# Optimization experiments

Measured on AMD Instinct MI355X. Metric: run time of the kernel, lower is better.

Reference implementation:

```python
import jax, jax.numpy as jnp
import numpy as np

B, T, H, W, C = 2, 8, 64, 64, 128
NH, KT, KH, KW = 4, 3, 7, 7
HD = C // NH
SCALE = HD ** -0.5


def _starts(L, ks):
    i = jnp.arange(L)
    return jnp.clip(i - ks // 2, 0, L - ks)  # NATTEN border-clamped window start


def _na3d(q, k, v, rpb):
    # q,k,v: [B,T,H,W,NH,HD]; rpb: [NH,2KT-1,2KH-1,2KW-1]
    st, sh, sw = _starts(T, KT), _starts(H, KH), _starts(W, KW)
    ot, oh, ow = jnp.meshgrid(jnp.arange(KT), jnp.arange(KH), jnp.arange(KW), indexing='ij')
    ot, oh, ow = ot.ravel(), oh.ravel(), ow.ravel()          # [K] kernel offsets, K=KT*KH*KW
    t_abs = st[None, :] + ot[:, None]                        # [K,T] absolute neighbor coords
    h_abs = sh[None, :] + oh[:, None]                        # [K,H]
    w_abs = sw[None, :] + ow[:, None]                        # [K,W]
    qs = q * SCALE
    it, ih, iw = jnp.arange(T), jnp.arange(H), jnp.arange(W)

    def score_step(_, idx):
        ta, ha, wa = idx
        kg = k[:, ta][:, :, ha][:, :, :, wa]                 # [B,T,H,W,NH,HD] shifted keys
        s = jnp.einsum('bthwnd,bthwnd->bthwn', qs, kg)
        rt = ta - it + (KT - 1)
        rh = ha - ih + (KH - 1)
        rw = wa - iw + (KW - 1)
        bias = rpb[:, rt][:, :, rh][:, :, :, rw]             # [NH,T,H,W]
        return None, s + jnp.transpose(bias, (1, 2, 3, 0))[None]

    _, scores = jax.lax.scan(score_step, None, (t_abs, h_abs, w_abs))  # [K,B,T,H,W,NH]
    attn = jax.nn.softmax(scores, axis=0)

    def av_step(acc, xs):
        a, ta, ha, wa = xs
        vg = v[:, ta][:, :, ha][:, :, :, wa]                 # [B,T,H,W,NH,HD]
        return acc + a[..., None] * vg, None

    out, _ = jax.lax.scan(av_step, jnp.zeros_like(q), (attn, t_abs, h_abs, w_abs))
    return out


def setup_inputs() -> dict:
    key = jax.random.key(0)
    ks = jax.random.split(key, 6)
    x = jax.random.normal(ks[0], (B, T, H, W, C), jnp.float32)
    y = jax.random.normal(ks[1], (B, T, H, W, C), jnp.float32)
    qv_w = jax.random.normal(ks[2], (C, 2 * C), jnp.float32) * 0.02
    qv_b = jnp.zeros((2 * C,), jnp.float32)
    k_w = jax.random.normal(ks[3], (C, C), jnp.float32) * 0.02
    k_b = jnp.zeros((C,), jnp.float32)
    proj_w = jax.random.normal(ks[4], (C, C), jnp.float32) * 0.02
    proj_b = jnp.zeros((C,), jnp.float32)
    rpb = jax.random.normal(ks[5], (NH, 2 * KT - 1, 2 * KH - 1, 2 * KW - 1), jnp.float32) * 0.02
    return {'x': x, 'y': y, 'qv_w': qv_w, 'qv_b': qv_b, 'k_w': k_w, 'k_b': k_b,
            'proj_w': proj_w, 'proj_b': proj_b, 'rpb': rpb}


def reference(x, y, qv_w, qv_b, k_w, k_b, proj_w, proj_b, rpb):
    qv = (x @ qv_w + qv_b).reshape(B, T, H, W, 2, NH, HD)
    q, v = qv[..., 0, :, :], qv[..., 1, :, :]
    k = (y @ k_w + k_b).reshape(B, T, H, W, NH, HD)
    o = _na3d(q, k, v, rpb).reshape(B, T, H, W, C)
    return o @ proj_w + proj_b
```

## Files before the change

kernel.cpp:

```cpp
#include <hip/hip_runtime.h>
#include <hip/hip_bf16.h>
#include <hip/hip_fp16.h>
#include <cmath>

#define Bv   2
#define Tv   8
#define Hv   64
#define Wv   64
#define MPOS (Bv*Tv*Hv*Wv)
#define SCALEv 0.17677669529663687f

#define SPOS  196
#define SVT   464
#define NCOLS 232

#define KOFF   0
#define VTOFF  13312
#define POFF   28160
#define RPBOFF 57856
#define INVOFF 61248
#define SCROFF 61504
#define SMEM_BYTES 69696

#define KPAD 136

typedef __attribute__((ext_vector_type(8))) short bf16x8;
typedef __attribute__((ext_vector_type(4))) float f32x4;

__device__ __forceinline__ unsigned short f2bf16(float x) {
  return __builtin_bit_cast(unsigned short, __float2bfloat16(x));
}
__device__ __forceinline__ float bf2f(unsigned short h) {
  return __uint_as_float((unsigned)h << 16);
}
__device__ __forceinline__ float h2f(unsigned short h) {
  return __half2float(__builtin_bit_cast(__half, h));
}
__device__ __forceinline__ unsigned short f2h(float x) {
  return __builtin_bit_cast(unsigned short, __float2half(x));
}
__device__ __forceinline__ unsigned pk2(float a, float b) {
  return (unsigned)f2bf16(a) | ((unsigned)f2bf16(b) << 16);
}
__device__ __forceinline__ void gload_lds16(const void* gsrc, void* ldst) {
  __builtin_amdgcn_global_load_lds(
      (const __attribute__((address_space(1))) unsigned int*)gsrc,
      (__attribute__((address_space(3))) unsigned int*)ldst, 16, 0, 0);
}

__global__ __launch_bounds__(256) void preconvert(
    const float* __restrict__ qv_w, const float* __restrict__ k_w,
    const float* __restrict__ proj_w,
    ushort* __restrict__ wqvT, ushort* __restrict__ wkT,
    ushort* __restrict__ wpT_hi, ushort* __restrict__ wpT_lo) {
  const int id = blockIdx.x * 256 + threadIdx.x;
  if (id < 32768) {
    const int n = id >> 7, kk = id & 127;
    wqvT[n * KPAD + kk] = f2bf16(qv_w[kk * 256 + n]);
  } else if (id < 49152) {
    const int j = id - 32768;
    const int n = j >> 7, kk = j & 127;
    wkT[n * KPAD + kk] = f2bf16(k_w[kk * 128 + n]);
  } else {
    const int j = id - 49152;
    const int n = j >> 7, kk = j & 127;
    const float v = proj_w[kk * 128 + n];
    const unsigned short hi = f2bf16(v);
    wpT_hi[n * KPAD + kk] = hi;
    wpT_lo[n * KPAD + kk] = f2bf16(v - bf2f(hi));
  }
}

__global__ __launch_bounds__(512) void gemm_qvk(
    const float* __restrict__ x, const float* __restrict__ y,
    const ushort* __restrict__ wqvT, const ushort* __restrict__ wkT,
    const float* __restrict__ qv_b, const float* __restrict__ k_b,
    ushort* __restrict__ qbuf, ushort* __restrict__ vbuf,
    ushort* __restrict__ kbuf) {
  __shared__ ushort Ws[128 * KPAD];
  const int tid  = threadIdx.x;
  const int bx   = blockIdx.x;
  const int seg  = bx >> 9;
  const int row0 = (bx & 511) * 128;

  const float*  A    = (seg == 2) ? y : x;
  const ushort* W    = (seg == 0) ? wqvT : (seg == 1) ? wqvT + 128 * KPAD : wkT;
  const float*  bias = (seg == 0) ? qv_b : (seg == 1) ? qv_b + 128 : k_b;
  ushort*       outp = (seg == 0) ? qbuf : (seg == 1) ? vbuf : kbuf;
  const float   scale = (seg == 0) ? SCALEv : 1.0f;

  {
    const uint4* wg = (const uint4*)W;
    for (int i = tid; i < 2176; i += 512)
      gload_lds16(wg + i, (uint4*)Ws + i);
  }

  const int wv = tid >> 6, lane = tid & 63, quad = lane >> 4, l16 = lane & 15;
  const int arow = row0 + wv * 16 + l16;

  bf16x8 af[4];
#pragma unroll
  for (int kk = 0; kk < 4; ++kk) {
    const float4* ap = (const float4*)(A + (size_t)arow * 128 + kk * 32 + quad * 8);
    const float4 a = ap[0], b2 = ap[1];
    af[kk] = __builtin_bit_cast(bf16x8,
        make_uint4(pk2(a.x, a.y), pk2(a.z, a.w), pk2(b2.x, b2.y), pk2(b2.z, b2.w)));
  }
  __syncthreads();

  f32x4 C[8];
#pragma unroll
  for (int nt = 0; nt < 8; ++nt) C[nt] = (f32x4){0.f, 0.f, 0.f, 0.f};

#pragma unroll
  for (int kk = 0; kk < 4; ++kk) {
#pragma unroll
    for (int nt = 0; nt < 8; ++nt) {
      const bf16x8 b2 = *(const bf16x8*)(Ws + (nt * 16 + l16) * KPAD + kk * 32 + quad * 8);
      C[nt] = __builtin_amdgcn_mfma_f32_16x16x32_bf16(af[kk], b2, C[nt], 0, 0, 0);
    }
  }

#pragma unroll
  for (int nt = 0; nt < 8; ++nt) {
    const int col = nt * 16 + l16;
    const float bv = bias[col];
#pragma unroll
    for (int r2 = 0; r2 < 4; ++r2) {
      const size_t row = row0 + wv * 16 + quad * 4 + r2;
      outp[row * 128 + col] = f2bf16((C[nt][r2] + bv) * scale);
    }
  }
}

__global__ __launch_bounds__(512) void gemm_proj_mfma(
    const float* __restrict__ o, const ushort* __restrict__ wpT_hi,
    const ushort* __restrict__ wpT_lo, const float* __restrict__ proj_b,
    float* __restrict__ out) {
  __shared__ ushort Wh[128 * KPAD];
  __shared__ ushort Wl[128 * KPAD];
  const int tid  = threadIdx.x;
  const int row0 = blockIdx.x * 128;
  {
    const uint4* wgh = (const uint4*)wpT_hi;
    const uint4* wgl = (const uint4*)wpT_lo;
    for (int i = tid; i < 2176; i += 512) {
      gload_lds16(wgh + i, (uint4*)Wh + i);
      gload_lds16(wgl + i, (uint4*)Wl + i);
    }
  }

  const int wv = tid >> 6, lane = tid & 63, quad = lane >> 4, l16 = lane & 15;
  const int arow = row0 + wv * 16 + l16;

  bf16x8 ah[4], al[4];
#pragma unroll
  for (int kk = 0; kk < 4; ++kk) {
    const float4* ap = (const float4*)(o + (size_t)arow * 128 + kk * 32 + quad * 8);
    const float4 a = ap[0], b2 = ap[1];
    const float vs[8] = {a.x, a.y, a.z, a.w, b2.x, b2.y, b2.z, b2.w};
    unsigned hw[4], lw[4];
#pragma unroll
    for (int e = 0; e < 4; ++e) {
      const unsigned short h0 = f2bf16(vs[2 * e]);
      const unsigned short h1 = f2bf16(vs[2 * e + 1]);
      hw[e] = (unsigned)h0 | ((unsigned)h1 << 16);
      lw[e] = (unsigned)f2bf16(vs[2 * e] - bf2f(h0)) |
              ((unsigned)f2bf16(vs[2 * e + 1] - bf2f(h1)) << 16);
    }
    ah[kk] = __builtin_bit_cast(bf16x8, make_uint4(hw[0], hw[1], hw[2], hw[3]));
    al[kk] = __builtin_bit_cast(bf16x8, make_uint4(lw[0], lw[1], lw[2], lw[3]));
  }
  __syncthreads();

  f32x4 C[8];
#pragma unroll
  for (int nt = 0; nt < 8; ++nt) C[nt] = (f32x4){0.f, 0.f, 0.f, 0.f};

#pragma unroll
  for (int kk = 0; kk < 4; ++kk) {
#pragma unroll
    for (int nt = 0; nt < 8; ++nt) {
      const int boff = (nt * 16 + l16) * KPAD + kk * 32 + quad * 8;
      const bf16x8 bh = *(const bf16x8*)(Wh + boff);
      const bf16x8 bl = *(const bf16x8*)(Wl + boff);
      C[nt] = __builtin_amdgcn_mfma_f32_16x16x32_bf16(ah[kk], bh, C[nt], 0, 0, 0);
      C[nt] = __builtin_amdgcn_mfma_f32_16x16x32_bf16(ah[kk], bl, C[nt], 0, 0, 0);
      C[nt] = __builtin_amdgcn_mfma_f32_16x16x32_bf16(al[kk], bh, C[nt], 0, 0, 0);
    }
  }

#pragma unroll
  for (int nt = 0; nt < 8; ++nt) {
    const int col = nt * 16 + l16;
    const float bv = proj_b[col];
#pragma unroll
    for (int r2 = 0; r2 < 4; ++r2) {
      const size_t row = row0 + wv * 16 + quad * 4 + r2;
      out[row * 128 + col] = C[nt][r2] + bv;
    }
  }
}

__global__ __launch_bounds__(1024, 8)
void na3d_tile(
    const ushort* __restrict__ qin,
    const ushort* __restrict__ kin,
    const ushort* __restrict__ vin,
    const float* __restrict__ rpb,
    float* __restrict__ oout) {
  __shared__ __align__(16) unsigned char smem[SMEM_BYTES];

  const int tid  = threadIdx.x;
  const int wv   = tid >> 6;
  const int lane = tid & 63;
  const int quad = lane >> 4;
  const int l16  = lane & 15;

  const int bx   = blockIdx.x;
  const int head = bx & 3;
  const int tile = bx >> 2;
  const int w0 = (tile & 7) << 3;
  const int h0 = ((tile >> 3) & 7) << 3;
  const int t  = (tile >> 6) & 7;
  const int b  = tile >> 9;

  const int st  = min(max(t - 1, 0), Tv - 3);
  const int u_h = min(max(h0 - 3, 0), Hv - 14);
  const int u_w = min(max(w0 - 3, 0), Wv - 14);
  const int rt_b = st - t + 2;

  const int mtile = wv & 3;
  bf16x8 afrag;
  {
    const int q_a  = mtile * 16 + l16;
    const int qh_a = h0 + (q_a >> 3), qw_a = w0 + (q_a & 7);
    const size_t qpos_a = ((size_t)(b * Tv + t) * Hv + qh_a) * Wv + qw_a;
    afrag = *(const bf16x8*)(qin + qpos_a * 128 + head * 32 + quad * 8);
  }
  if (tid < 845) ((float*)(smem + RPBOFF))[tid] = rpb[head * 845 + tid];

  const int qs = tid >> 4, l16s = tid & 15;
  const int qh_s = h0 + (qs >> 3), qw_s = w0 + (qs & 7);
  const int sh_s = min(max(qh_s - 3, 0), Hv - 7);
  const int sw_s = min(max(qw_s - 3, 0), Wv - 7);
  const int dh_s = sh_s - u_h, dw_s = sw_s - u_w;
  const int rh0 = sh_s - qh_s + 6, rw0 = sw_s - qw_s + 6;

  const int khalf = wv >> 3, mtA = (wv >> 1) & 3, ntA = wv & 1;
  const int dcol = ntA * 16 + l16;
  const unsigned vsw = ((unsigned)(dcol >> 3) & 3u) << 5;

  const int vpos = tid >> 2, vc = tid & 3;
  const int vrh = vpos / 14, vrw = vpos - vrh * 14;
  const size_t vsp = ((size_t)(u_h + vrh) * Wv + (u_w + vrw)) * 16 + head * 4 + vc;
  const int km = wv * 64 + lane;
  const int kpos0 = min(km >> 2, SPOS - 1);
  const int kslot = km & 3;
  const int kc = (kslot - (kpos0 >> 2)) & 3;
  const int krh = kpos0 / 14, krw = kpos0 - krh * 14;
  const size_t ksp = ((size_t)(u_h + krh) * Wv + (u_w + krw)) * 16 + head * 4 + kc;

  f32x4 o = {0.f, 0.f, 0.f, 0.f};
  float sum = 0.f;
  uint4 vv;

  {
    const size_t tbase = (size_t)(b * Tv + st) * Hv * Wv * 16;
    if (tid < SPOS * 4) vv = ((const uint4*)vin)[tbase + vsp];
    if (wv < 13)
      gload_lds16((const uint4*)kin + tbase + ksp,
                  smem + KOFF + wv * 1024 + lane * 16);
  }

#pragma unroll 1
  for (int pass = 0; pass < 3; ++pass) {
    if (tid < SPOS * 4) {
      const unsigned sw = (unsigned)vc << 5;
      const unsigned v4[4] = {vv.x, vv.y, vv.z, vv.w};
#pragma unroll
      for (int m2 = 0; m2 < 4; ++m2) {
        const int d0 = 8 * vc + 2 * m2;
        const unsigned base = (unsigned)d0 * SVT + (unsigned)vpos * 2;
        *(ushort*)(smem + VTOFF + (base ^ sw))         = (ushort)(v4[m2] & 0xffffu);
        *(ushort*)(smem + VTOFF + ((base + SVT) ^ sw)) = (ushort)(v4[m2] >> 16);
      }
    }
    if (pass == 0 && tid < 576) {
      const int d = tid / 18, jj = tid - d * 18;
      const unsigned base = (unsigned)d * SVT + 392u + (unsigned)jj * 4;
      *(unsigned*)(smem + VTOFF + (base ^ (((unsigned)d >> 3) << 5))) = 0u;
    }
    __syncthreads();

    {
      ushort* ph = (ushort*)(smem + POFF);
      for (int nt = (wv >> 2); nt < 13; nt += 4) {
        const int u = nt * 16 + l16;
        const int slot = (quad + (u >> 2)) & 3;
        const bf16x8 bfrag = *(const bf16x8*)(smem + KOFF + u * 64 + slot * 16);
        f32x4 c = {0.f, 0.f, 0.f, 0.f};
        c = __builtin_amdgcn_mfma_f32_16x16x32_bf16(afrag, bfrag, c, 0, 0, 0);
#pragma unroll
        for (int r2 = 0; r2 < 4; ++r2) {
          const int qrow = mtile * 16 + quad * 4 + r2;
          ph[qrow * NCOLS + u] = f2h(c[r2]);
        }
      }
    }
    __syncthreads();

    {
      const ushort* Ps = (const ushort*)(smem + POFF) + qs * NCOLS;
      const float* rpb_l = (const float*)(smem + RPBOFF) + (rt_b + pass) * 169;
      float ex[4];
      int uu[4];
#pragma unroll
      for (int k = 0; k < 4; ++k) {
        const int e = l16s + 16 * k;
        const int a = (e * 37) >> 8;
        const int bb = e - 7 * a;
        uu[k] = (dh_s + a) * 14 + dw_s + bb;
        if (e < 49) {
          const float s = h2f(Ps[uu[k]]) + rpb_l[(rh0 + a) * 13 + rw0 + bb];
          ex[k] = __expf(s);
          sum += ex[k];
        }
      }
      if (pass == 2) {
        float sm = sum;
        sm += __shfl_xor(sm, 1);
        sm += __shfl_xor(sm, 2);
        sm += __shfl_xor(sm, 4);
        sm += __shfl_xor(sm, 8);
        if (l16s == 0) ((float*)(smem + INVOFF))[qs] = 1.0f / sm;
      }
      __builtin_amdgcn_sched_barrier(0);
      {
        uint4* Pv = (uint4*)(smem + POFF + (size_t)qs * SVT);
        Pv[l16s] = make_uint4(0u, 0u, 0u, 0u);
        if (l16s < 13) Pv[l16s + 16] = make_uint4(0u, 0u, 0u, 0u);
      }
      __builtin_amdgcn_sched_barrier(0);
      ushort* Pr = (ushort*)(smem + POFF) + qs * NCOLS;
#pragma unroll
      for (int k = 0; k < 4; ++k) {
        const int e = l16s + 16 * k;
        if (e < 49) Pr[uu[k]] = f2bf16(ex[k]);
      }
    }
    __syncthreads();

    if (pass < 2) {
      const size_t tbase = (size_t)(b * Tv + st + pass + 1) * Hv * Wv * 16;
      if (tid < SPOS * 4) vv = ((const uint4*)vin)[tbase + vsp];
      if (wv < 13)
        gload_lds16((const uint4*)kin + tbase + ksp,
                    smem + KOFF + wv * 1024 + lane * 16);
    }

    {
      const unsigned char* Abase = smem + POFF + (size_t)(mtA * 16 + l16) * SVT;
      const unsigned vlocal = (unsigned)dcol * SVT;
      const int kt0 = khalf ? 4 : 0;
      const int kt1 = khalf ? 7 : 4;
      for (int kt = kt0; kt < kt1; ++kt) {
        const bf16x8 a  = *(const bf16x8*)(Abase + kt * 64 + quad * 16);
        const bf16x8 bb = *(const bf16x8*)(smem + VTOFF +
                            ((vlocal + kt * 64 + quad * 16) ^ vsw));
        o = __builtin_amdgcn_mfma_f32_16x16x32_bf16(a, bb, o, 0, 0, 0);
      }
    }
    if (pass < 2) __syncthreads();
  }

  {
    f32x4* part = (f32x4*)(smem + SCROFF);
    if (khalf) part[(wv & 7) * 64 + lane] = o;
    __syncthreads();
    if (!khalf) {
      const f32x4 p2 = part[wv * 64 + lane];
      const float* invArr = (const float*)(smem + INVOFF);
#pragma unroll
      for (int r2 = 0; r2 < 4; ++r2) {
        const int qrow = mtA * 16 + quad * 4 + r2;
        const float val = (o[r2] + p2[r2]) * invArr[qrow];
        const int qh2 = h0 + (qrow >> 3), qw2 = w0 + (qrow & 7);
        const size_t qp2 = ((size_t)(b * Tv + t) * Hv + qh2) * Wv + qw2;
        oout[qp2 * 128 + head * 32 + dcol] = val;
      }
    }
  }
}

extern "C" void kernel_launch(void* const* d_in, const int* in_sizes, int n_in,
                              void* d_out, int out_size, void* d_ws, size_t ws_size,
                              hipStream_t stream) {
  const float* x      = (const float*)d_in[0];
  const float* y      = (const float*)d_in[1];
  const float* qv_w   = (const float*)d_in[2];
  const float* qv_b   = (const float*)d_in[3];
  const float* k_w    = (const float*)d_in[4];
  const float* k_b    = (const float*)d_in[5];
  const float* proj_w = (const float*)d_in[6];
  const float* proj_b = (const float*)d_in[7];
  const float* rpb    = (const float*)d_in[8];
  float* out = (float*)d_out;

  const size_t elems = (size_t)MPOS * 128;
  ushort* qbuf = (ushort*)d_ws;
  ushort* kbuf = qbuf + elems;
  ushort* vbuf = kbuf + elems;
  float*  obuf = (float*)(vbuf + elems);
  ushort* wqvT   = (ushort*)(obuf + elems);
  ushort* wkT    = wqvT + 256 * KPAD;
  ushort* wpT_hi = wkT + 128 * KPAD;
  ushort* wpT_lo = wpT_hi + 128 * KPAD;

  preconvert    <<<256,  256, 0, stream>>>(qv_w, k_w, proj_w, wqvT, wkT, wpT_hi, wpT_lo);
  gemm_qvk      <<<1536, 512, 0, stream>>>(x, y, wqvT, wkT, qv_b, k_b, qbuf, vbuf, kbuf);
  na3d_tile     <<<4096, 1024, 0, stream>>>(qbuf, kbuf, vbuf, rpb, obuf);
  gemm_proj_mfma<<<512,  512, 0, stream>>>(obuf, wpT_hi, wpT_lo, proj_b, out);
}
```

Measured before the change: 258.2 us.

## Split QVK GEMM into fused QV and K kernels; widen attention epilogue

Measured after the change: 284.6 us. 10.2% more time.

```diff
diff --git a/kernel.cpp b/kernel.cpp
--- a/kernel.cpp
+++ b/kernel.cpp
@@ -20,7 +20,7 @@
 #define RPBOFF 57856
 #define INVOFF 61248
 #define SCROFF 61504
-#define SMEM_BYTES 69696
+#define SMEM_BYTES 77888
 
 #define KPAD 136
 
@@ -71,27 +71,17 @@
   }
 }
 
-__global__ __launch_bounds__(512) void gemm_qvk(
-    const float* __restrict__ x, const float* __restrict__ y,
-    const ushort* __restrict__ wqvT, const ushort* __restrict__ wkT,
-    const float* __restrict__ qv_b, const float* __restrict__ k_b,
-    ushort* __restrict__ qbuf, ushort* __restrict__ vbuf,
-    ushort* __restrict__ kbuf) {
-  __shared__ ushort Ws[128 * KPAD];
+__global__ __launch_bounds__(512) void gemm_qv(
+    const float* __restrict__ x, const ushort* __restrict__ wqvT,
+    const float* __restrict__ qv_b,
+    ushort* __restrict__ qbuf, ushort* __restrict__ vbuf) {
+  __shared__ ushort Ws[256 * KPAD];
   const int tid  = threadIdx.x;
-  const int bx   = blockIdx.x;
-  const int seg  = bx >> 9;
-  const int row0 = (bx & 511) * 128;
-
-  const float*  A    = (seg == 2) ? y : x;
-  const ushort* W    = (seg == 0) ? wqvT : (seg == 1) ? wqvT + 128 * KPAD : wkT;
-  const float*  bias = (seg == 0) ? qv_b : (seg == 1) ? qv_b + 128 : k_b;
-  ushort*       outp = (seg == 0) ? qbuf : (seg == 1) ? vbuf : kbuf;
-  const float   scale = (seg == 0) ? SCALEv : 1.0f;
-
-  {
-    const uint4* wg = (const uint4*)W;
-    for (int i = tid; i < 2176; i += 512)
+  const int row0 = blockIdx.x * 128;
+
+  {
+    const uint4* wg = (const uint4*)wqvT;
+    for (int i = tid; i < 4352; i += 512)
       gload_lds16(wg + i, (uint4*)Ws + i);
   }
 
@@ -101,13 +91,66 @@
   bf16x8 af[4];
 #pragma unroll
   for (int kk = 0; kk < 4; ++kk) {
-    const float4* ap = (const float4*)(A + (size_t)arow * 128 + kk * 32 + quad * 8);
+    const float4* ap = (const float4*)(x + (size_t)arow * 128 + kk * 32 + quad * 8);
     const float4 a = ap[0], b2 = ap[1];
     af[kk] = __builtin_bit_cast(bf16x8,
         make_uint4(pk2(a.x, a.y), pk2(a.z, a.w), pk2(b2.x, b2.y), pk2(b2.z, b2.w)));
   }
   __syncthreads();
 
+  f32x4 C[16];
+#pragma unroll
+  for (int nt = 0; nt < 16; ++nt) C[nt] = (f32x4){0.f, 0.f, 0.f, 0.f};
+
+#pragma unroll
+  for (int kk = 0; kk < 4; ++kk) {
+#pragma unroll
+    for (int nt = 0; nt < 16; ++nt) {
+      const bf16x8 b2 = *(const bf16x8*)(Ws + (nt * 16 + l16) * KPAD + kk * 32 + quad * 8);
+      C[nt] = __builtin_amdgcn_mfma_f32_16x16x32_bf16(af[kk], b2, C[nt], 0, 0, 0);
+    }
+  }
+
+#pragma unroll
+  for (int nt = 0; nt < 16; ++nt) {
+    const int col = nt * 16 + l16;
+    const float bv = qv_b[col];
+#pragma unroll
+    for (int r2 = 0; r2 < 4; ++r2) {
+      const size_t row = row0 + wv * 16 + quad * 4 + r2;
+      const float val = C[nt][r2] + bv;
+      if (col < 128) qbuf[row * 128 + col] = f2bf16(val * SCALEv);
+      else           vbuf[row * 128 + (col - 128)] = f2bf16(val);
+    }
+  }
+}
+
+__global__ __launch_bounds__(512) void gemm_k(
+    const float* __restrict__ y, const ushort* __restrict__ wkT,
+    const float* __restrict__ k_b, ushort* __restrict__ kbuf) {
+  __shared__ ushort Ws[128 * KPAD];
+  const int tid  = threadIdx.x;
+  const int row0 = blockIdx.x * 128;
+
+  {
+    const uint4* wg = (const uint4*)wkT;
+    for (int i = tid; i < 2176; i += 512)
+      gload_lds16(wg + i, (uint4*)Ws + i);
+  }
+
+  const int wv = tid >> 6, lane = tid & 63, quad = lane >> 4, l16 = lane & 15;
+  const int arow = row0 + wv * 16 + l16;
+
+  bf16x8 af[4];
+#pragma unroll
+  for (int kk = 0; kk < 4; ++kk) {
+    const float4* ap = (const float4*)(y + (size_t)arow * 128 + kk * 32 + quad * 8);
+    const float4 a = ap[0], b2 = ap[1];
+    af[kk] = __builtin_bit_cast(bf16x8,
+        make_uint4(pk2(a.x, a.y), pk2(a.z, a.w), pk2(b2.x, b2.y), pk2(b2.z, b2.w)));
+  }
+  __syncthreads();
+
   f32x4 C[8];
 #pragma unroll
   for (int nt = 0; nt < 8; ++nt) C[nt] = (f32x4){0.f, 0.f, 0.f, 0.f};
@@ -124,11 +167,11 @@
 #pragma unroll
   for (int nt = 0; nt < 8; ++nt) {
     const int col = nt * 16 + l16;
-    const float bv = bias[col];
+    const float bv = k_b[col];
 #pragma unroll
     for (int r2 = 0; r2 < 4; ++r2) {
       const size_t row = row0 + wv * 16 + quad * 4 + r2;
-      outp[row * 128 + col] = f2bf16((C[nt][r2] + bv) * scale);
+      kbuf[row * 128 + col] = f2bf16(C[nt][r2] + bv);
     }
   }
 }
@@ -376,19 +419,21 @@
 
   {
     f32x4* part = (f32x4*)(smem + SCROFF);
-    if (khalf) part[(wv & 7) * 64 + lane] = o;
+    part[wv * 64 + lane] = o;
     __syncthreads();
-    if (!khalf) {
-      const f32x4 p2 = part[wv * 64 + lane];
-      const float* invArr = (const float*)(smem + INVOFF);
-#pragma unroll
-      for (int r2 = 0; r2 < 4; ++r2) {
-        const int qrow = mtA * 16 + quad * 4 + r2;
-        const float val = (o[r2] + p2[r2]) * invArr[qrow];
-        const int qh2 = h0 + (qrow >> 3), qw2 = w0 + (qrow & 7);
-        const size_t qp2 = ((size_t)(b * Tv + t) * Hv + qh2) * Wv + qw2;
-        oout[qp2 * 128 + head * 32 + dcol] = val;
-      }
+    const float* pf = (const float*)(smem + SCROFF);
+    const float* invArr = (const float*)(smem + INVOFF);
+    const int colw = lane & 31;
+    const int nt2 = colw >> 4, l16w = colw & 15;
+#pragma unroll
+    for (int i = 0; i < 2; ++i) {
+      const int q = 4 * wv + 2 * i + (lane >> 5);
+      const int mt = q >> 4, qd = (q >> 2) & 3, r2 = q & 3;
+      const int idx0 = (((mt * 2 + nt2) * 64) + qd * 16 + l16w) * 4 + r2;
+      const float val = (pf[idx0] + pf[idx0 + 2048]) * invArr[q];
+      const int qh2 = h0 + (q >> 3), qw2 = w0 + (q & 7);
+      const size_t qp2 = ((size_t)(b * Tv + t) * Hv + qh2) * Wv + qw2;
+      oout[qp2 * 128 + head * 32 + colw] = val;
     }
   }
 }
@@ -418,7 +463,8 @@
   ushort* wpT_lo = wpT_hi + 128 * KPAD;
 
   preconvert    <<<256,  256, 0, stream>>>(qv_w, k_w, proj_w, wqvT, wkT, wpT_hi, wpT_lo);
-  gemm_qvk      <<<1536, 512, 0, stream>>>(x, y, wqvT, wkT, qv_b, k_b, qbuf, vbuf, kbuf);
+  gemm_qv       <<<512,  512, 0, stream>>>(x, wqvT, qv_b, qbuf, vbuf);
+  gemm_k        <<<512,  512, 0, stream>>>(y, wkT, k_b, kbuf);
   na3d_tile     <<<4096, 1024, 0, stream>>>(qbuf, kbuf, vbuf, rpb, obuf);
   gemm_proj_mfma<<<512,  512, 0, stream>>>(obuf, wpT_hi, wpT_lo, proj_b, out);
 }
```

## Use head-major Q/K/V/O layout and fuse Q and V projection blocks

Applied to the files above, without the earlier changes.

Measured after the change: 335.5 us. 29.9% more time.

```diff
diff --git a/kernel.cpp b/kernel.cpp
--- a/kernel.cpp
+++ b/kernel.cpp
@@ -20,7 +20,7 @@
 #define RPBOFF 57856
 #define INVOFF 61248
 #define SCROFF 61504
-#define SMEM_BYTES 69696
+#define SMEM_BYTES 77888
 
 #define KPAD 136
 
@@ -77,21 +77,17 @@
     const float* __restrict__ qv_b, const float* __restrict__ k_b,
     ushort* __restrict__ qbuf, ushort* __restrict__ vbuf,
     ushort* __restrict__ kbuf) {
-  __shared__ ushort Ws[128 * KPAD];
+  __shared__ ushort Ws[256 * KPAD];
   const int tid  = threadIdx.x;
   const int bx   = blockIdx.x;
-  const int seg  = bx >> 9;
+  const bool isK = (bx >= 512);
   const int row0 = (bx & 511) * 128;
 
-  const float*  A    = (seg == 2) ? y : x;
-  const ushort* W    = (seg == 0) ? wqvT : (seg == 1) ? wqvT + 128 * KPAD : wkT;
-  const float*  bias = (seg == 0) ? qv_b : (seg == 1) ? qv_b + 128 : k_b;
-  ushort*       outp = (seg == 0) ? qbuf : (seg == 1) ? vbuf : kbuf;
-  const float   scale = (seg == 0) ? SCALEv : 1.0f;
-
+  const float* A = isK ? y : x;
   {
-    const uint4* wg = (const uint4*)W;
-    for (int i = tid; i < 2176; i += 512)
+    const uint4* wg = (const uint4*)(isK ? wkT : wqvT);
+    const int nW = isK ? 2176 : 4352;
+    for (int i = tid; i < nW; i += 512)
       gload_lds16(wg + i, (uint4*)Ws + i);
   }
 
@@ -108,27 +104,35 @@
   }
   __syncthreads();
 
-  f32x4 C[8];
-#pragma unroll
-  for (int nt = 0; nt < 8; ++nt) C[nt] = (f32x4){0.f, 0.f, 0.f, 0.f};
-
-#pragma unroll
-  for (int kk = 0; kk < 4; ++kk) {
-#pragma unroll
-    for (int nt = 0; nt < 8; ++nt) {
+  const int NT = isK ? 8 : 16;
+  f32x4 C[16];
+#pragma unroll
+  for (int nt = 0; nt < 16; ++nt) C[nt] = (f32x4){0.f, 0.f, 0.f, 0.f};
+
+  for (int nt = 0; nt < NT; ++nt) {
+#pragma unroll
+    for (int kk = 0; kk < 4; ++kk) {
       const bf16x8 b2 = *(const bf16x8*)(Ws + (nt * 16 + l16) * KPAD + kk * 32 + quad * 8);
       C[nt] = __builtin_amdgcn_mfma_f32_16x16x32_bf16(af[kk], b2, C[nt], 0, 0, 0);
     }
   }
 
-#pragma unroll
-  for (int nt = 0; nt < 8; ++nt) {
+  for (int nt = 0; nt < NT; ++nt) {
     const int col = nt * 16 + l16;
-    const float bv = bias[col];
+    const float bv = isK ? k_b[col] : qv_b[col];
 #pragma unroll
     for (int r2 = 0; r2 < 4; ++r2) {
       const size_t row = row0 + wv * 16 + quad * 4 + r2;
-      outp[row * 128 + col] = f2bf16((C[nt][r2] + bv) * scale);
+      const float val = C[nt][r2] + bv;
+      if (isK) {
+        kbuf[(size_t)(col >> 5) * MPOS * 32 + row * 32 + (col & 31)] = f2bf16(val);
+      } else if (col < 128) {
+        qbuf[(size_t)(col >> 5) * MPOS * 32 + row * 32 + (col & 31)] =
+            f2bf16(val * SCALEv);
+      } else {
+        const int vc2 = col - 128;
+        vbuf[(size_t)(vc2 >> 5) * MPOS * 32 + row * 32 + (vc2 & 31)] = f2bf16(val);
+      }
     }
   }
 }
@@ -156,7 +160,8 @@
   bf16x8 ah[4], al[4];
 #pragma unroll
   for (int kk = 0; kk < 4; ++kk) {
-    const float4* ap = (const float4*)(o + (size_t)arow * 128 + kk * 32 + quad * 8);
+    const float4* ap =
+        (const float4*)(o + (size_t)kk * MPOS * 32 + (size_t)arow * 32 + quad * 8);
     const float4 a = ap[0], b2 = ap[1];
     const float vs[8] = {a.x, a.y, a.z, a.w, b2.x, b2.y, b2.z, b2.w};
     unsigned hw[4], lw[4];
@@ -230,13 +235,18 @@
   const int u_w = min(max(w0 - 3, 0), Wv - 14);
   const int rt_b = st - t + 2;
 
+  const ushort* qin_h = qin + (size_t)head * MPOS * 32;
+  const uint4*  kin_h = (const uint4*)kin + (size_t)head * MPOS * 4;
+  const uint4*  vin_h = (const uint4*)vin + (size_t)head * MPOS * 4;
+  float*        oout_h = oout + (size_t)head * MPOS * 32;
+
   const int mtile = wv & 3;
   bf16x8 afrag;
   {
     const int q_a  = mtile * 16 + l16;
     const int qh_a = h0 + (q_a >> 3), qw_a = w0 + (q_a & 7);
     const size_t qpos_a = ((size_t)(b * Tv + t) * Hv + qh_a) * Wv + qw_a;
-    afrag = *(const bf16x8*)(qin + qpos_a * 128 + head * 32 + quad * 8);
+    afrag = *(const bf16x8*)(qin_h + qpos_a * 32 + quad * 8);
   }
   if (tid < 845) ((float*)(smem + RPBOFF))[tid] = rpb[head * 845 + tid];
 
@@ -253,24 +263,23 @@
 
   const int vpos = tid >> 2, vc = tid & 3;
   const int vrh = vpos / 14, vrw = vpos - vrh * 14;
-  const size_t vsp = ((size_t)(u_h + vrh) * Wv + (u_w + vrw)) * 16 + head * 4 + vc;
+  const size_t vsp = ((size_t)(u_h + vrh) * Wv + (u_w + vrw)) * 4 + vc;
   const int km = wv * 64 + lane;
   const int kpos0 = min(km >> 2, SPOS - 1);
   const int kslot = km & 3;
   const int kc = (kslot - (kpos0 >> 2)) & 3;
   const int krh = kpos0 / 14, krw = kpos0 - krh * 14;
-  const size_t ksp = ((size_t)(u_h + krh) * Wv + (u_w + krw)) * 16 + head * 4 + kc;
+  const size_t ksp = ((size_t)(u_h + krh) * Wv + (u_w + krw)) * 4 + kc;
 
   f32x4 o = {0.f, 0.f, 0.f, 0.f};
   float sum = 0.f;
   uint4 vv;
 
   {
-    const size_t tbase = (size_t)(b * Tv + st) * Hv * Wv * 16;
-    if (tid < SPOS * 4) vv = ((const uint4*)vin)[tbase + vsp];
+    const size_t tbase = (size_t)(b * Tv + st) * Hv * Wv * 4;
+    if (tid < SPOS * 4) vv = vin_h[tbase + vsp];
     if (wv < 13)
-      gload_lds16((const uint4*)kin + tbase + ksp,
-                  smem + KOFF + wv * 1024 + lane * 16);
+      gload_lds16(kin_h + tbase + ksp, smem + KOFF + wv * 1024 + lane * 16);
   }
 
 #pragma unroll 1
@@ -352,11 +361,10 @@
     __syncthreads();
 
     if (pass < 2) {
-      const size_t tbase = (size_t)(b * Tv + st + pass + 1) * Hv * Wv * 16;
-      if (tid < SPOS * 4) vv = ((const uint4*)vin)[tbase + vsp];
+      const size_t tbase = (size_t)(b * Tv + st + pass + 1) * Hv * Wv * 4;
+      if (tid < SPOS * 4) vv = vin_h[tbase + vsp];
       if (wv < 13)
-        gload_lds16((const uint4*)kin + tbase + ksp,
-                    smem + KOFF + wv * 1024 + lane * 16);
+        gload_lds16(kin_h + tbase + ksp, smem + KOFF + wv * 1024 + lane * 16);
     }
 
     {
@@ -376,19 +384,21 @@
 
   {
     f32x4* part = (f32x4*)(smem + SCROFF);
-    if (khalf) part[(wv & 7) * 64 + lane] = o;
+    part[wv * 64 + lane] = o;
     __syncthreads();
-    if (!khalf) {
-      const f32x4 p2 = part[wv * 64 + lane];
-      const float* invArr = (const float*)(smem + INVOFF);
-#pragma unroll
-      for (int r2 = 0; r2 < 4; ++r2) {
-        const int qrow = mtA * 16 + quad * 4 + r2;
-        const float val = (o[r2] + p2[r2]) * invArr[qrow];
-        const int qh2 = h0 + (qrow >> 3), qw2 = w0 + (qrow & 7);
-        const size_t qp2 = ((size_t)(b * Tv + t) * Hv + qh2) * Wv + qw2;
-        oout[qp2 * 128 + head * 32 + dcol] = val;
-      }
+    const float* pf = (const float*)(smem + SCROFF);
+    const float* invArr = (const float*)(smem + INVOFF);
+    const int colw = lane & 31;
+    const int nt2 = colw >> 4, l16w = colw & 15;
+#pragma unroll
+    for (int i = 0; i < 2; ++i) {
+      const int q = 4 * wv + 2 * i + (lane >> 5);
+      const int mt = q >> 4, qd = (q >> 2) & 3, r2 = q & 3;
+      const int idx0 = (((mt * 2 + nt2) * 64) + qd * 16 + l16w) * 4 + r2;
+      const float val = (pf[idx0] + pf[idx0 + 2048]) * invArr[q];
+      const int qh2 = h0 + (q >> 3), qw2 = w0 + (q & 7);
+      const size_t qp2 = ((size_t)(b * Tv + t) * Hv + qh2) * Wv + qw2;
+      oout_h[qp2 * 32 + colw] = val;
     }
   }
 }
@@ -418,7 +428,7 @@
   ushort* wpT_lo = wpT_hi + 128 * KPAD;
 
   preconvert    <<<256,  256, 0, stream>>>(qv_w, k_w, proj_w, wqvT, wkT, wpT_hi, wpT_lo);
-  gemm_qvk      <<<1536, 512, 0, stream>>>(x, y, wqvT, wkT, qv_b, k_b, qbuf, vbuf, kbuf);
+  gemm_qvk      <<<1024, 512, 0, stream>>>(x, y, wqvT, wkT, qv_b, k_b, qbuf, vbuf, kbuf);
   na3d_tile     <<<4096, 1024, 0, stream>>>(qbuf, kbuf, vbuf, rpb, obuf);
   gemm_proj_mfma<<<512,  512, 0, stream>>>(obuf, wpT_hi, wpT_lo, proj_b, out);
 }
```

## Store Q/K/V and attention output head-major and halve attention block size

Applied to the files above, without the earlier changes.

After: 242.3 us. -6.2%, faster.

```diff
diff --git a/kernel.cpp b/kernel.cpp
--- a/kernel.cpp
+++ b/kernel.cpp
@@ -19,8 +19,7 @@
 #define POFF   28160
 #define RPBOFF 57856
 #define INVOFF 61248
-#define SCROFF 61504
-#define SMEM_BYTES 69696
+#define SMEM_BYTES 61504
 
 #define KPAD 136
 
@@ -128,7 +127,8 @@
 #pragma unroll
     for (int r2 = 0; r2 < 4; ++r2) {
       const size_t row = row0 + wv * 16 + quad * 4 + r2;
-      outp[row * 128 + col] = f2bf16((C[nt][r2] + bv) * scale);
+      outp[(size_t)(col >> 5) * MPOS * 32 + row * 32 + (col & 31)] =
+          f2bf16((C[nt][r2] + bv) * scale);
     }
   }
 }
@@ -156,7 +156,8 @@
   bf16x8 ah[4], al[4];
 #pragma unroll
   for (int kk = 0; kk < 4; ++kk) {
-    const float4* ap = (const float4*)(o + (size_t)arow * 128 + kk * 32 + quad * 8);
+    const float4* ap =
+        (const float4*)(o + (size_t)kk * MPOS * 32 + (size_t)arow * 32 + quad * 8);
     const float4 a = ap[0], b2 = ap[1];
     const float vs[8] = {a.x, a.y, a.z, a.w, b2.x, b2.y, b2.z, b2.w};
     unsigned hw[4], lw[4];
@@ -202,7 +203,7 @@
   }
 }
 
-__global__ __launch_bounds__(1024, 8)
+__global__ __launch_bounds__(512, 4)
 void na3d_tile(
     const ushort* __restrict__ qin,
     const ushort* __restrict__ kin,
@@ -230,72 +231,99 @@
   const int u_w = min(max(w0 - 3, 0), Wv - 14);
   const int rt_b = st - t + 2;
 
+  const ushort* qin_h = qin + (size_t)head * MPOS * 32;
+  const uint4*  kin_h = (const uint4*)kin + (size_t)head * MPOS * 4;
+  const uint4*  vin_h = (const uint4*)vin + (size_t)head * MPOS * 4;
+
   const int mtile = wv & 3;
   bf16x8 afrag;
   {
     const int q_a  = mtile * 16 + l16;
     const int qh_a = h0 + (q_a >> 3), qw_a = w0 + (q_a & 7);
     const size_t qpos_a = ((size_t)(b * Tv + t) * Hv + qh_a) * Wv + qw_a;
-    afrag = *(const bf16x8*)(qin + qpos_a * 128 + head * 32 + quad * 8);
-  }
-  if (tid < 845) ((float*)(smem + RPBOFF))[tid] = rpb[head * 845 + tid];
-
-  const int qs = tid >> 4, l16s = tid & 15;
+    afrag = *(const bf16x8*)(qin_h + qpos_a * 32 + quad * 8);
+  }
+  {
+    float r0 = 0.f, r1 = 0.f;
+    if (tid < 845) r0 = rpb[head * 845 + tid];
+    if (tid < 333) r1 = rpb[head * 845 + tid + 512];
+    if (tid < 845) ((float*)(smem + RPBOFF))[tid] = r0;
+    if (tid < 333) ((float*)(smem + RPBOFF))[tid + 512] = r1;
+  }
+
+  const int qs = tid >> 3, l8s = tid & 7;
   const int qh_s = h0 + (qs >> 3), qw_s = w0 + (qs & 7);
   const int sh_s = min(max(qh_s - 3, 0), Hv - 7);
   const int sw_s = min(max(qw_s - 3, 0), Wv - 7);
   const int dh_s = sh_s - u_h, dw_s = sw_s - u_w;
   const int rh0 = sh_s - qh_s + 6, rw0 = sw_s - qw_s + 6;
 
-  const int khalf = wv >> 3, mtA = (wv >> 1) & 3, ntA = wv & 1;
+  const int mtA = wv >> 1, ntA = wv & 1;
   const int dcol = ntA * 16 + l16;
   const unsigned vsw = ((unsigned)(dcol >> 3) & 3u) << 5;
 
-  const int vpos = tid >> 2, vc = tid & 3;
-  const int vrh = vpos / 14, vrw = vpos - vrh * 14;
-  const size_t vsp = ((size_t)(u_h + vrh) * Wv + (u_w + vrw)) * 16 + head * 4 + vc;
-  const int km = wv * 64 + lane;
-  const int kpos0 = min(km >> 2, SPOS - 1);
-  const int kslot = km & 3;
-  const int kc = (kslot - (kpos0 >> 2)) & 3;
-  const int krh = kpos0 / 14, krw = kpos0 - krh * 14;
-  const size_t ksp = ((size_t)(u_h + krh) * Wv + (u_w + krw)) * 16 + head * 4 + kc;
-
   f32x4 o = {0.f, 0.f, 0.f, 0.f};
   float sum = 0.f;
-  uint4 vv;
-
-  {
-    const size_t tbase = (size_t)(b * Tv + st) * Hv * Wv * 16;
-    if (tid < SPOS * 4) vv = ((const uint4*)vin)[tbase + vsp];
-    if (wv < 13)
-      gload_lds16((const uint4*)kin + tbase + ksp,
-                  smem + KOFF + wv * 1024 + lane * 16);
+  uint4 vv0, vv1;
+
+  const int vp0 = tid >> 2, vc0 = tid & 3;
+  const int vr0 = vp0 / 14;
+  const unsigned vsp0 = ((u_h + vr0) * Wv + (u_w + (vp0 - vr0 * 14))) * 4 + vc0;
+  const int j1 = tid + 512;
+  const int vp1 = j1 >> 2, vc1 = j1 & 3;
+  const int vr1 = vp1 / 14;
+  const unsigned vsp1 = ((u_h + vr1) * Wv + (u_w + (vp1 - vr1 * 14))) * 4 + vc1;
+
+  {
+    const unsigned tbase = (unsigned)(b * Tv + st) * (Hv * Wv * 4);
+    vv0 = vin_h[tbase + vsp0];
+    if (tid < 272) vv1 = vin_h[tbase + vsp1];
+    for (int ch = wv; ch < 13; ch += 8) {
+      const int m = ch * 64 + lane;
+      const int pos = min(m >> 2, SPOS - 1);
+      const int c = ((m & 3) - (pos >> 2)) & 3;
+      const int rh = pos / 14;
+      const unsigned sp = ((u_h + rh) * Wv + (u_w + (pos - rh * 14))) * 4 + c;
+      gload_lds16(kin_h + tbase + sp, smem + KOFF + ch * 1024 + lane * 16);
+    }
   }
 
 #pragma unroll 1
   for (int pass = 0; pass < 3; ++pass) {
-    if (tid < SPOS * 4) {
-      const unsigned sw = (unsigned)vc << 5;
-      const unsigned v4[4] = {vv.x, vv.y, vv.z, vv.w};
+    {
+      const unsigned sw0 = (unsigned)vc0 << 5;
+      const unsigned v4[4] = {vv0.x, vv0.y, vv0.z, vv0.w};
 #pragma unroll
       for (int m2 = 0; m2 < 4; ++m2) {
-        const int d0 = 8 * vc + 2 * m2;
-        const unsigned base = (unsigned)d0 * SVT + (unsigned)vpos * 2;
-        *(ushort*)(smem + VTOFF + (base ^ sw))         = (ushort)(v4[m2] & 0xffffu);
-        *(ushort*)(smem + VTOFF + ((base + SVT) ^ sw)) = (ushort)(v4[m2] >> 16);
-      }
-    }
-    if (pass == 0 && tid < 576) {
-      const int d = tid / 18, jj = tid - d * 18;
-      const unsigned base = (unsigned)d * SVT + 392u + (unsigned)jj * 4;
-      *(unsigned*)(smem + VTOFF + (base ^ (((unsigned)d >> 3) << 5))) = 0u;
+        const int d0 = 8 * vc0 + 2 * m2;
+        const unsigned base = (unsigned)d0 * SVT + (unsigned)vp0 * 2;
+        *(ushort*)(smem + VTOFF + (base ^ sw0))         = (ushort)(v4[m2] & 0xffffu);
+        *(ushort*)(smem + VTOFF + ((base + SVT) ^ sw0)) = (ushort)(v4[m2] >> 16);
+      }
+      if (tid < 272) {
+        const unsigned sw1 = (unsigned)vc1 << 5;
+        const unsigned w4[4] = {vv1.x, vv1.y, vv1.z, vv1.w};
+#pragma unroll
+        for (int m2 = 0; m2 < 4; ++m2) {
+          const int d0 = 8 * vc1 + 2 * m2;
+          const unsigned base = (unsigned)d0 * SVT + (unsigned)vp1 * 2;
+          *(ushort*)(smem + VTOFF + (base ^ sw1))         = (ushort)(w4[m2] & 0xffffu);
+          *(ushort*)(smem + VTOFF + ((base + SVT) ^ sw1)) = (ushort)(w4[m2] >> 16);
+        }
+      }
+    }
+    if (pass == 0) {
+      for (int i = tid; i < 576; i += 512) {
+        const int d = i / 18, jj = i - d * 18;
+        const unsigned base = (unsigned)d * SVT + 392u + (unsigned)jj * 4;
+        *(unsigned*)(smem + VTOFF + (base ^ (((unsigned)d >> 3) << 5))) = 0u;
+      }
     }
     __syncthreads();
 
     {
       ushort* ph = (ushort*)(smem + POFF);
-      for (int nt = (wv >> 2); nt < 13; nt += 4) {
+      for (int nt = (wv >> 2); nt < 13; nt += 2) {
         const int u = nt * 16 + l16;
         const int slot = (quad + (u >> 2)) & 3;
         const bf16x8 bfrag = *(const bf16x8*)(smem + KOFF + u * 64 + slot * 16);
@@ -313,11 +341,11 @@
     {
       const ushort* Ps = (const ushort*)(smem + POFF) + qs * NCOLS;
       const float* rpb_l = (const float*)(smem + RPBOFF) + (rt_b + pass) * 169;
-      float ex[4];
-      int uu[4];
-#pragma unroll
-      for (int k = 0; k < 4; ++k) {
-        const int e = l16s + 16 * k;
+      float ex[7];
+      int uu[7];
+#pragma unroll
+      for (int k = 0; k < 7; ++k) {
+        const int e = l8s + 8 * k;
         const int a = (e * 37) >> 8;
         const int bb = e - 7 * a;
         uu[k] = (dh_s + a) * 14 + dw_s + bb;
@@ -332,39 +360,46 @@
         sm += __shfl_xor(sm, 1);
         sm += __shfl_xor(sm, 2);
         sm += __shfl_xor(sm, 4);
-        sm += __shfl_xor(sm, 8);
-        if (l16s == 0) ((float*)(smem + INVOFF))[qs] = 1.0f / sm;
+        if (l8s == 0) ((float*)(smem + INVOFF))[qs] = 1.0f / sm;
       }
       __builtin_amdgcn_sched_barrier(0);
       {
         uint4* Pv = (uint4*)(smem + POFF + (size_t)qs * SVT);
-        Pv[l16s] = make_uint4(0u, 0u, 0u, 0u);
-        if (l16s < 13) Pv[l16s + 16] = make_uint4(0u, 0u, 0u, 0u);
+#pragma unroll
+        for (int c = 0; c < 4; ++c) {
+          const int idx = l8s + 8 * c;
+          if (idx < 29) Pv[idx] = make_uint4(0u, 0u, 0u, 0u);
+        }
       }
       __builtin_amdgcn_sched_barrier(0);
       ushort* Pr = (ushort*)(smem + POFF) + qs * NCOLS;
 #pragma unroll
-      for (int k = 0; k < 4; ++k) {
-        const int e = l16s + 16 * k;
+      for (int k = 0; k < 7; ++k) {
+        const int e = l8s + 8 * k;
         if (e < 49) Pr[uu[k]] = f2bf16(ex[k]);
       }
     }
     __syncthreads();
 
     if (pass < 2) {
-      const size_t tbase = (size_t)(b * Tv + st + pass + 1) * Hv * Wv * 16;
-      if (tid < SPOS * 4) vv = ((const uint4*)vin)[tbase + vsp];
-      if (wv < 13)
-        gload_lds16((const uint4*)kin + tbase + ksp,
-                    smem + KOFF + wv * 1024 + lane * 16);
+      const unsigned tbase = (unsigned)(b * Tv + st + pass + 1) * (Hv * Wv * 4);
+      vv0 = vin_h[tbase + vsp0];
+      if (tid < 272) vv1 = vin_h[tbase + vsp1];
+      for (int ch = wv; ch < 13; ch += 8) {
+        const int m = ch * 64 + lane;
+        const int pos = min(m >> 2, SPOS - 1);
+        const int c = ((m & 3) - (pos >> 2)) & 3;
+        const int rh = pos / 14;
+        const unsigned sp = ((u_h + rh) * Wv + (u_w + (pos - rh * 14))) * 4 + c;
+        gload_lds16(kin_h + tbase + sp, smem + KOFF + ch * 1024 + lane * 16);
+      }
     }
 
     {
       const unsigned char* Abase = smem + POFF + (size_t)(mtA * 16 + l16) * SVT;
       const unsigned vlocal = (unsigned)dcol * SVT;
-      const int kt0 = khalf ? 4 : 0;
-      const int kt1 = khalf ? 7 : 4;
-      for (int kt = kt0; kt < kt1; ++kt) {
+#pragma unroll
+      for (int kt = 0; kt < 7; ++kt) {
         const bf16x8 a  = *(const bf16x8*)(Abase + kt * 64 + quad * 16);
         const bf16x8 bb = *(const bf16x8*)(smem + VTOFF +
                             ((vlocal + kt * 64 + quad * 16) ^ vsw));
@@ -375,20 +410,15 @@
   }
 
   {
-    f32x4* part = (f32x4*)(smem + SCROFF);
-    if (khalf) part[(wv & 7) * 64 + lane] = o;
-    __syncthreads();
-    if (!khalf) {
-      const f32x4 p2 = part[wv * 64 + lane];
-      const float* invArr = (const float*)(smem + INVOFF);
-#pragma unroll
-      for (int r2 = 0; r2 < 4; ++r2) {
-        const int qrow = mtA * 16 + quad * 4 + r2;
-        const float val = (o[r2] + p2[r2]) * invArr[qrow];
-        const int qh2 = h0 + (qrow >> 3), qw2 = w0 + (qrow & 7);
-        const size_t qp2 = ((size_t)(b * Tv + t) * Hv + qh2) * Wv + qw2;
-        oout[qp2 * 128 + head * 32 + dcol] = val;
-      }
+    float* oout_h = oout + (size_t)head * MPOS * 32;
+    const float* invArr = (const float*)(smem + INVOFF);
+#pragma unroll
+    for (int r2 = 0; r2 < 4; ++r2) {
+      const int qrow = mtA * 16 + quad * 4 + r2;
+      const float val = o[r2] * invArr[qrow];
+      const int qh2 = h0 + (qrow >> 3), qw2 = w0 + (qrow & 7);
+      const size_t qp2 = ((size_t)(b * Tv + t) * Hv + qh2) * Wv + qw2;
+      oout_h[qp2 * 32 + dcol] = val;
     }
   }
 }
@@ -419,6 +449,6 @@
 
   preconvert    <<<256,  256, 0, stream>>>(qv_w, k_w, proj_w, wqvT, wkT, wpT_hi, wpT_lo);
   gemm_qvk      <<<1536, 512, 0, stream>>>(x, y, wqvT, wkT, qv_b, k_b, qbuf, vbuf, kbuf);
-  na3d_tile     <<<4096, 1024, 0, stream>>>(qbuf, kbuf, vbuf, rpb, obuf);
+  na3d_tile     <<<4096, 512, 0, stream>>>(qbuf, kbuf, vbuf, rpb, obuf);
   gemm_proj_mfma<<<512,  512, 0, stream>>>(obuf, wpT_hi, wpT_lo, proj_b, out);
 }
```
